# Performance work log

Measured on AMD Instinct MI355X. Metric: run time of the kernel, lower is better.

Reference implementation:

```python
import jax, jax.numpy as jnp
import numpy as np

D_MODEL = 1024
NUM_HEADS = 16
D_K = D_MODEL // NUM_HEADS
SCALE = 1.0 / np.sqrt(D_K).astype(np.float32)


def _rope_cos_sin(T, d_k):
    inv_freq = 1.0 / (10000.0 ** (jnp.arange(0, d_k, 2, dtype=jnp.float32) / d_k))
    t = jnp.arange(T, dtype=jnp.float32)
    freqs = jnp.outer(t, inv_freq)                      # [T, d_k/2]
    emb = jnp.concatenate([freqs, freqs], axis=-1)      # [T, d_k]
    return jnp.cos(emb)[None, None], jnp.sin(emb)[None, None]  # [1,1,T,d_k]


def _rotate_half(x):
    x1, x2 = x[..., : x.shape[-1] // 2], x[..., x.shape[-1] // 2 :]
    return jnp.concatenate([-x2, x1], axis=-1)


def setup_inputs() -> dict:
    key = jax.random.key(0)
    ks = jax.random.split(key, 8)
    B, T, C = 2, 2048, D_MODEL
    x = jax.random.normal(ks[0], (B, T, C), dtype=jnp.float32)
    # torch nn.Linear weights are [out, in]; forward does x @ W.T
    s = 1.0 / np.sqrt(C)
    Wq = jax.random.uniform(ks[1], (C, C), jnp.float32, -s, s)
    Wk = jax.random.uniform(ks[2], (C, C), jnp.float32, -s, s)
    Wv = jax.random.uniform(ks[3], (C, C), jnp.float32, -s, s)
    Wo = jax.random.uniform(ks[4], (C, C), jnp.float32, -s, s)
    bo = jax.random.uniform(ks[5], (C,), jnp.float32, -s, s)
    sector_bias = jnp.zeros((1, NUM_HEADS, 1, 1), dtype=jnp.float32)
    sector_weights = jax.random.uniform(ks[6], (B, T), jnp.float32, 0.5, 1.5)
    # causal mask, broadcastable to [B,H,T,T]; 0 -> masked
    mask = jnp.tril(jnp.ones((T, T), dtype=jnp.int32))[None, None]
    return {
        "x": x, "Wq": Wq, "Wk": Wk, "Wv": Wv, "Wo": Wo, "bo": bo,
        "sector_bias": sector_bias, "sector_weights": sector_weights,
        "mask": mask,
    }


def reference(x, Wq, Wk, Wv, Wo, bo, sector_bias, sector_weights, mask):
    B, T, C = x.shape
    H, dk = NUM_HEADS, D_K
    q = (x @ Wq.T).reshape(B, T, H, dk).transpose(0, 2, 1, 3)  # [B,H,T,dk]
    k = (x @ Wk.T).reshape(B, T, H, dk).transpose(0, 2, 1, 3)
    v = (x @ Wv.T).reshape(B, T, H, dk).transpose(0, 2, 1, 3)
    cos, sin = _rope_cos_sin(T, dk)
    q = q * cos + _rotate_half(q) * sin
    k = k * cos + _rotate_half(k) * sin
    scores = jnp.einsum("bhqd,bhkd->bhqk", q, k) * SCALE
    scores = scores + sector_bias
    scores = scores * sector_weights[:, None, None, :]  # broadcast over key dim
    scores = jnp.where(mask == 0, -jnp.inf, scores)
    attn = jax.nn.softmax(scores, axis=-1)
    out = jnp.einsum("bhqk,bhkd->bhqd", attn, v)
    out = out.transpose(0, 2, 1, 3).reshape(B, T, C)
    return out @ Wo.T + bo
```

## Files before the change

### kernel.cpp

```cpp
#include <hip/hip_runtime.h>


typedef __bf16 bf16x8 __attribute__((ext_vector_type(8)));
typedef float f32x4 __attribute__((ext_vector_type(4)));
typedef float f32x16 __attribute__((ext_vector_type(16)));
typedef unsigned short u16x8 __attribute__((ext_vector_type(8)));

__device__ __forceinline__ unsigned short f2bf(float f) {
    union { float f; unsigned int u; } c; c.f = f;
    unsigned int u = c.u;
    unsigned int r = u + 0x7fffu + ((u >> 16) & 1u);
    return (unsigned short)(r >> 16);
}
__device__ __forceinline__ unsigned cvtpk(float lo, float hi) {
    unsigned r;
    asm("v_cvt_pk_bf16_f32 %0, %1, %2" : "=v"(r) : "v"(lo), "v"(hi));
    return r;
}
__device__ __forceinline__ void plswap(unsigned a, unsigned b, unsigned& r0, unsigned& r1) {
#if __has_builtin(__builtin_amdgcn_permlane32_swap)
    auto s = __builtin_amdgcn_permlane32_swap(a, b, false, false);
    r0 = (unsigned)s[0]; r1 = (unsigned)s[1];
#else
    const int hh = (int)(threadIdx.x & 63) >> 5;
    const unsigned oa = (unsigned)__shfl_xor((int)a, 32);
    const unsigned ob = (unsigned)__shfl_xor((int)b, 32);
    r0 = hh ? ob : a;
    r1 = hh ? b : oa;
#endif
}
__device__ __forceinline__ void stage8_f32(unsigned short* dst, const float* src) {
    const float4 a = *(const float4*)src;
    const float4 b = *(const float4*)(src + 4);
    u16x8 v;
    v[0] = f2bf(a.x); v[1] = f2bf(a.y); v[2] = f2bf(a.z); v[3] = f2bf(a.w);
    v[4] = f2bf(b.x); v[5] = f2bf(b.y); v[6] = f2bf(b.z); v[7] = f2bf(b.w);
    *(u16x8*)dst = v;
}
__device__ __forceinline__ void async16(const unsigned short* g, unsigned short* l) {
    __builtin_amdgcn_global_load_lds(
        (const __attribute__((address_space(1))) void*)g,
        (__attribute__((address_space(3))) void*)l, 16, 0, 0);
}

__global__ __launch_bounds__(256) void cvt_all(
    const float* __restrict__ x, const float* __restrict__ Wq, const float* __restrict__ Wk,
    const float* __restrict__ Wv, const float* __restrict__ Wo,
    unsigned short* __restrict__ dst, int hasX, int n8)
{
    const int i = blockIdx.x * 256 + threadIdx.x;
    if (i >= n8) return;
    int r = i;
    const float* src; int off;
    const int xg = hasX ? 524288 : 0;
    if (r < xg) { src = x; off = r; }
    else {
        r -= xg;
        const int w = r >> 17, o = r & 131071;
        src = (w == 0) ? Wq : (w == 1) ? Wk : (w == 2) ? Wv : Wo;
        off = o;
    }
    stage8_f32(&dst[(size_t)i * 8], &src[(size_t)off * 8]);
}

template<int A_BF16>
__global__ __launch_bounds__(256) void gemm_qkv(
    const void* __restrict__ Av, const unsigned short* __restrict__ Wb,
    unsigned short* __restrict__ outv, const float* __restrict__ swg)
{
    constexpr int K = 1024, BK = 32;
    __shared__ __align__(16) unsigned short As[128 * BK];
    __shared__ __align__(16) unsigned short Bs[128 * BK];
    const int tid = threadIdx.x;
    const int wid = tid >> 6, lane = tid & 63, g = lane >> 4, l = lane & 15;
    const int wm = (wid & 1) * 64, wn = (wid >> 1) * 64;
    const int m0 = blockIdx.y * 128, n0 = blockIdx.x * 128;
    const int z = blockIdx.z;
    const unsigned short* W = Wb + (size_t)z * 1048576;

    f32x4 acc[4][4];
#pragma unroll
    for (int i = 0; i < 4; ++i)
#pragma unroll
        for (int j = 0; j < 4; ++j) acc[i][j] = f32x4{0.f, 0.f, 0.f, 0.f};

    const int r = tid >> 2;
    const int c = (tid & 3) * 8;
    unsigned short* AsW = &As[wid * 512];
    unsigned short* BsW = &Bs[wid * 512];

    for (int k0 = 0; k0 < K; k0 += BK) {
        __syncthreads();
        if (A_BF16) {
            const unsigned short* A = (const unsigned short*)Av;
            async16(&A[(size_t)(m0 + r) * K + k0 + c], AsW);
            async16(&A[(size_t)(m0 + 64 + r) * K + k0 + c], AsW + 2048);
        } else {
            const float* A = (const float*)Av;
            stage8_f32(&As[tid * 8],        &A[(size_t)(m0 + r) * K + k0 + c]);
            stage8_f32(&As[tid * 8 + 2048], &A[(size_t)(m0 + 64 + r) * K + k0 + c]);
        }
        async16(&W[(size_t)(n0 + r) * K + k0 + c], BsW);
        async16(&W[(size_t)(n0 + 64 + r) * K + k0 + c], BsW + 2048);
        __syncthreads();

        bf16x8 af[4], bfr[4];
#pragma unroll
        for (int im = 0; im < 4; ++im) af[im]  = *(const bf16x8*)&As[(wm + im * 16 + l) * BK + g * 8];
#pragma unroll
        for (int in = 0; in < 4; ++in) bfr[in] = *(const bf16x8*)&Bs[(wn + in * 16 + l) * BK + g * 8];
#pragma unroll
        for (int im = 0; im < 4; ++im)
#pragma unroll
            for (int in = 0; in < 4; ++in)
                acc[im][in] = __builtin_amdgcn_mfma_f32_16x16x32_bf16(af[im], bfr[in], acc[im][in], 0, 0, 0);
    }

    unsigned short* outq = outv + (size_t)z * 4194304;
    if (z < 2) {
        float freq[2];
#pragma unroll
        for (int in = 0; in < 2; ++in)
            freq[in] = exp2f(-(float)(in * 16 + l) * 0.41524101186f);
#pragma unroll
        for (int im = 0; im < 4; ++im)
#pragma unroll
            for (int i = 0; i < 4; ++i) {
                const int m = m0 + wm + im * 16 + g * 4 + i;
                const int b = m >> 11, t = m & 2047;
                float fw = 1.0f;
                if (z == 1) fw = 0.18033688011f * swg[(b << 11) + t];
#pragma unroll
                for (int in = 0; in < 2; ++in) {
                    const int n = n0 + wn + in * 16 + l;
                    const int h = n >> 6, d = n & 63;
                    const float ang = (float)t * freq[in];
                    const float cs = __cosf(ang), sn = __sinf(ang);
                    const float x1 = acc[im][in][i], x2 = acc[im][in + 2][i];
                    const size_t bidx = (((size_t)b * 16 + h) * 2048 + t) << 6;
                    outq[bidx + d]      = f2bf((x1 * cs - x2 * sn) * fw);
                    outq[bidx + d + 32] = f2bf((x2 * cs + x1 * sn) * fw);
                }
            }
    } else {
#pragma unroll
        for (int im = 0; im < 4; ++im)
#pragma unroll
            for (int in = 0; in < 4; ++in) {
                const int n = n0 + wn + in * 16 + l;
                const int h = n >> 6, d = n & 63;
                const int mb = m0 + wm + im * 16 + g * 4;
                const int bq = mb >> 11, t0 = mb & 2047;
                ushort4 pk;
                pk.x = f2bf(acc[im][in][0]); pk.y = f2bf(acc[im][in][1]);
                pk.z = f2bf(acc[im][in][2]); pk.w = f2bf(acc[im][in][3]);
                *(ushort4*)&outq[((size_t)(bq * 16 + h)) * 131072 + (size_t)d * 2048 + t0] = pk;
            }
    }
}

__global__ __launch_bounds__(256) void gemm_proj(
    const unsigned short* __restrict__ A, const unsigned short* __restrict__ W,
    float* __restrict__ out, const float* __restrict__ bias)
{
    constexpr int K = 1024, BK = 32;
    __shared__ __align__(16) unsigned short As[64 * BK];
    __shared__ __align__(16) unsigned short Bs[128 * BK];
    const int tid = threadIdx.x;
    const int wid = tid >> 6, lane = tid & 63, g = lane >> 4, l = lane & 15;
    const int wm = (wid & 1) * 32, wn = (wid >> 1) * 64;
    const int m0 = blockIdx.y * 64, n0 = blockIdx.x * 128;

    f32x4 acc[2][4];
#pragma unroll
    for (int i = 0; i < 2; ++i)
#pragma unroll
        for (int j = 0; j < 4; ++j) acc[i][j] = f32x4{0.f, 0.f, 0.f, 0.f};

    const int r = tid >> 2;
    const int c = (tid & 3) * 8;
    unsigned short* AsW = &As[wid * 512];
    unsigned short* BsW = &Bs[wid * 512];

    for (int k0 = 0; k0 < K; k0 += BK) {
        __syncthreads();
        async16(&A[(size_t)(m0 + r) * K + k0 + c], AsW);
        async16(&W[(size_t)(n0 + r) * K + k0 + c], BsW);
        async16(&W[(size_t)(n0 + 64 + r) * K + k0 + c], BsW + 2048);
        __syncthreads();

        bf16x8 af[2], bfr[4];
#pragma unroll
        for (int im = 0; im < 2; ++im) af[im]  = *(const bf16x8*)&As[(wm + im * 16 + l) * BK + g * 8];
#pragma unroll
        for (int in = 0; in < 4; ++in) bfr[in] = *(const bf16x8*)&Bs[(wn + in * 16 + l) * BK + g * 8];
#pragma unroll
        for (int im = 0; im < 2; ++im)
#pragma unroll
            for (int in = 0; in < 4; ++in)
                acc[im][in] = __builtin_amdgcn_mfma_f32_16x16x32_bf16(af[im], bfr[in], acc[im][in], 0, 0, 0);
    }

#pragma unroll
    for (int im = 0; im < 2; ++im)
#pragma unroll
        for (int in = 0; in < 4; ++in) {
            const int n = n0 + wn + in * 16 + l;
#pragma unroll
            for (int i = 0; i < 4; ++i) {
                const int m = m0 + wm + im * 16 + g * 4 + i;
                out[(size_t)m * 1024 + n] = acc[im][in][i] + bias[n];
            }
        }
}

__global__ __launch_bounds__(128, 2) void flash_attn(
    const unsigned short* __restrict__ Q, const unsigned short* __restrict__ Kg,
    const unsigned short* __restrict__ VT, const float* __restrict__ sbias,
    const float* __restrict__ sw, unsigned short* __restrict__ attn)
{
    constexpr int T = 2048;
    __shared__ __align__(16) unsigned short Mem[64 * 72 * 2];
    unsigned short* Ks  = Mem;
    unsigned short* VsT = Mem + 64 * 72;
    float* Cmb = (float*)Mem;

    const int tid = threadIdx.x, wid = tid >> 6, lane = tid & 63;
    const int hl = lane & 31, hh = lane >> 5;
    const int id = blockIdx.x;
    const int p  = 63 - (id >> 5);
    const int bh = id & 31, b = bh >> 4, h = bh & 15;
    const size_t base = (size_t)bh * T * 64;
    const size_t vtb  = (size_t)bh * 64 * T;
    const float bias = sbias[h];
    const float* swb = sw + b * T;

    bf16x8 onef;
#pragma unroll
    for (int j = 0; j < 8; ++j) onef[j] = (__bf16)1.0f;

    const int q0 = p * 32;
    bf16x8 qf[4];
#pragma unroll
    for (int ks = 0; ks < 4; ++ks)
        qf[ks] = *(const bf16x8*)&Q[base + (size_t)(q0 + hl) * 64 + ks * 16 + hh * 8];

    f32x16 oacc[2], lrow;
#pragma unroll
    for (int r = 0; r < 16; ++r) { oacc[0][r] = 0.f; oacc[1][r] = 0.f; lrow[r] = 0.f; }

    u16x8 kpre[4], vpre[4];
#pragma unroll
    for (int s = 0; s < 4; ++s) {
        const int ci = s * 128 + tid, rr = ci >> 3, c8 = (ci & 7) * 8;
        kpre[s] = *(const u16x8*)&Kg[base + (size_t)rr * 64 + c8];
        vpre[s] = *(const u16x8*)&VT[vtb + (size_t)rr * T + c8];
    }

    const int rounds = (p + 2) >> 1;
    for (int rd = 0; rd < rounds; ++rd) {
        const int k0 = rd * 64;
        __syncthreads();
#pragma unroll
        for (int s = 0; s < 4; ++s) {
            const int ci = s * 128 + tid, rr = ci >> 3, c8 = (ci & 7) * 8;
            *(u16x8*)&Ks[rr * 72 + c8]  = kpre[s];
            *(u16x8*)&VsT[rr * 72 + c8] = vpre[s];
        }
        __syncthreads();
        if (rd + 1 < rounds) {
            const int k1 = k0 + 64;
#pragma unroll
            for (int s = 0; s < 4; ++s) {
                const int ci = s * 128 + tid, rr = ci >> 3, c8 = (ci & 7) * 8;
                kpre[s] = *(const u16x8*)&Kg[base + (size_t)(k1 + rr) * 64 + c8];
                vpre[s] = *(const u16x8*)&VT[vtb + (size_t)rr * T + k1 + c8];
            }
        }

        const int kw0 = k0 + wid * 32;
        if (kw0 <= q0 + 31) {
            f32x16 sx;
#pragma unroll
            for (int r = 0; r < 16; ++r) sx[r] = 0.f;
#pragma unroll
            for (int ks = 0; ks < 4; ++ks) {
                const bf16x8 kf = *(const bf16x8*)&Ks[(wid * 32 + hl) * 72 + ks * 16 + hh * 8];
                sx = __builtin_amdgcn_mfma_f32_32x32x16_bf16(kf, qf[ks], sx, 0, 0, 0);
            }
            if (bias != 0.0f) {
                const float bn = bias * 1.44269504f;
#pragma unroll
                for (int r = 0; r < 16; ++r) {
                    const int kl = (r & 3) + 8 * (r >> 2) + 4 * hh;
                    sx[r] += bn * swb[kw0 + kl];
                }
            }
            if (kw0 + 31 > q0) {
                const int dq = q0 + hl - kw0;
#pragma unroll
                for (int r = 0; r < 16; ++r) {
                    const int kl = (r & 3) + 8 * (r >> 2) + 4 * hh;
                    sx[r] = (kl <= dq) ? sx[r] : -1e30f;
                }
            }
#pragma unroll
            for (int r = 0; r < 16; ++r) sx[r] = exp2f(sx[r]);

            unsigned wds[8];
#pragma unroll
            for (int g2 = 0; g2 < 4; ++g2) {
                wds[g2 * 2]     = cvtpk(sx[g2 * 4],     sx[g2 * 4 + 1]);
                wds[g2 * 2 + 1] = cvtpk(sx[g2 * 4 + 2], sx[g2 * 4 + 3]);
            }
            bf16x8 pf[2];
#pragma unroll
            for (int ks = 0; ks < 2; ++ks) {
                unsigned a0, a1, b0, b1;
                plswap(wds[4 * ks],     wds[4 * ks + 2], a0, a1);
                plswap(wds[4 * ks + 1], wds[4 * ks + 3], b0, b1);
                union { unsigned u[4]; bf16x8 v; } pk_;
                pk_.u[0] = a0; pk_.u[1] = b0;
                pk_.u[2] = a1; pk_.u[3] = b1;
                pf[ks] = pk_.v;
            }

            lrow = __builtin_amdgcn_mfma_f32_32x32x16_bf16(pf[0], onef, lrow, 0, 0, 0);
            lrow = __builtin_amdgcn_mfma_f32_32x32x16_bf16(pf[1], onef, lrow, 0, 0, 0);

#pragma unroll
            for (int ks = 0; ks < 2; ++ks)
#pragma unroll
                for (int dt = 0; dt < 2; ++dt) {
                    const bf16x8 vf = *(const bf16x8*)&VsT[(dt * 32 + hl) * 72 + wid * 32 + ks * 16 + hh * 8];
                    oacc[dt] = __builtin_amdgcn_mfma_f32_32x32x16_bf16(pf[ks], vf, oacc[dt], 0, 0, 0);
                }
        }
    }

    __syncthreads();
    if (wid == 1) {
#pragma unroll
        for (int dt = 0; dt < 2; ++dt)
#pragma unroll
            for (int r = 0; r < 16; ++r) Cmb[(dt * 16 + r) * 64 + lane] = oacc[dt][r];
#pragma unroll
        for (int r = 0; r < 16; ++r) Cmb[2048 + r * 64 + lane] = lrow[r];
    }
    __syncthreads();
    if (wid == 0) {
#pragma unroll
        for (int r = 0; r < 16; ++r) {
            const float li = 1.0f / (lrow[r] + Cmb[2048 + r * 64 + lane]);
            const int row = (r & 3) + 8 * (r >> 2) + 4 * hh;
            const int qr = q0 + row;
#pragma unroll
            for (int dt = 0; dt < 2; ++dt) {
                const float ov = oacc[dt][r] + Cmb[(dt * 16 + r) * 64 + lane];
                attn[(size_t)(b * T + qr) * 1024 + h * 64 + dt * 32 + hl] = f2bf(ov * li);
            }
        }
    }
}

extern "C" void kernel_launch(void* const* d_in, const int* in_sizes, int n_in,
                              void* d_out, int out_size, void* d_ws, size_t ws_size,
                              hipStream_t stream) {
    const float* x  = (const float*)d_in[0];
    const float* Wq = (const float*)d_in[1];
    const float* Wk = (const float*)d_in[2];
    const float* Wv = (const float*)d_in[3];
    const float* Wo = (const float*)d_in[4];
    const float* bo = (const float*)d_in[5];
    const float* sb = (const float*)d_in[6];
    const float* sw = (const float*)d_in[7];

    const size_t QKV_SZ = 4194304;
    const size_t W_SZ   = 1048576;
    unsigned short* ws16 = (unsigned short*)d_ws;
    const bool big = ws_size >= 2 * (4 * QKV_SZ + 4 * W_SZ);

    if (big) {
        unsigned short* xb    = ws16;
        unsigned short* Wb3   = xb + QKV_SZ;
        unsigned short* Wob   = Wb3 + 3 * W_SZ;
        unsigned short* qkv   = Wob + W_SZ;
        unsigned short* attnb = xb;

        cvt_all<<<4096, 256, 0, stream>>>(x, Wq, Wk, Wv, Wo, xb, 1, 1048576);
        gemm_qkv<1><<<dim3(8, 32, 3), 256, 0, stream>>>(xb, Wb3, qkv, sw);
        flash_attn<<<2048, 128, 0, stream>>>(qkv, qkv + QKV_SZ, qkv + 2 * QKV_SZ,
                                             sb, sw, attnb);
        gemm_proj<<<dim3(8, 64), 256, 0, stream>>>(attnb, Wob, (float*)d_out, bo);
    } else {
        unsigned short* qkv   = ws16;
        unsigned short* attnb = qkv + 3 * QKV_SZ;
        unsigned short* Wb3   = attnb;
        unsigned short* Wob   = qkv;

        cvt_all<<<1536, 256, 0, stream>>>(x, Wq, Wk, Wv, Wo, Wb3, 0, 393216);
        gemm_qkv<0><<<dim3(8, 32, 3), 256, 0, stream>>>(x, Wb3, qkv, sw);
        flash_attn<<<2048, 128, 0, stream>>>(qkv, qkv + QKV_SZ, qkv + 2 * QKV_SZ,
                                             sb, sw, attnb);
        cvt_all<<<512, 256, 0, stream>>>(x, Wo, Wo, Wo, Wo, Wob, 0, 131072);
        gemm_proj<<<dim3(8, 64), 256, 0, stream>>>(attnb, Wob, (float*)d_out, bo);
    }
}
```

Measured before the change: 205.8 us.

## Double-buffer LDS in QKV and projection GEMMs and remap blocks for XCD locality

Both GEMM kernels now use two LDS buffers, so the next K-tile is staged while MFMAs run on the current tile, leaving one barrier per iteration instead of two. Block indices are also remapped so that consecutive hardware-dispatched workgroups (round-robined across the 8 XCDs) land on neighbouring tiles, which should improve L2 reuse within each XCD. The cost is double the LDS footprint, which may reduce occupancy. With async loads, correctness depends on the vmcnt wait inside async16 and the barrier ordering.

```diff
diff --git a/kernel.cpp b/kernel.cpp
--- a/kernel.cpp
+++ b/kernel.cpp
@@ -69,13 +69,17 @@
     unsigned short* __restrict__ outv, const float* __restrict__ swg)
 {
     constexpr int K = 1024, BK = 32;
-    __shared__ __align__(16) unsigned short As[128 * BK];
-    __shared__ __align__(16) unsigned short Bs[128 * BK];
+    __shared__ __align__(16) unsigned short As[2][128 * BK];
+    __shared__ __align__(16) unsigned short Bs[2][128 * BK];
     const int tid = threadIdx.x;
     const int wid = tid >> 6, lane = tid & 63, g = lane >> 4, l = lane & 15;
     const int wm = (wid & 1) * 64, wn = (wid >> 1) * 64;
-    const int m0 = blockIdx.y * 128, n0 = blockIdx.x * 128;
-    const int z = blockIdx.z;
+
+    const int lin = blockIdx.x + (blockIdx.y << 3) + (blockIdx.z << 8);
+    const int wg  = (lin & 7) * 96 + (lin >> 3);
+    const int bx = wg & 7, by = (wg >> 3) & 31, bz = wg >> 8;
+    const int m0 = by * 128, n0 = bx * 128;
+    const int z = bz;
     const unsigned short* W = Wb + (size_t)z * 1048576;
 
     f32x4 acc[4][4];
@@ -86,34 +90,43 @@
 
     const int r = tid >> 2;
     const int c = (tid & 3) * 8;
-    unsigned short* AsW = &As[wid * 512];
-    unsigned short* BsW = &Bs[wid * 512];
-
-    for (int k0 = 0; k0 < K; k0 += BK) {
-        __syncthreads();
+
+    auto stage = [&](int buf, int k0) {
         if (A_BF16) {
             const unsigned short* A = (const unsigned short*)Av;
+            unsigned short* AsW = &As[buf][wid * 512];
             async16(&A[(size_t)(m0 + r) * K + k0 + c], AsW);
             async16(&A[(size_t)(m0 + 64 + r) * K + k0 + c], AsW + 2048);
         } else {
             const float* A = (const float*)Av;
-            stage8_f32(&As[tid * 8],        &A[(size_t)(m0 + r) * K + k0 + c]);
-            stage8_f32(&As[tid * 8 + 2048], &A[(size_t)(m0 + 64 + r) * K + k0 + c]);
-        }
+            stage8_f32(&As[buf][tid * 8],        &A[(size_t)(m0 + r) * K + k0 + c]);
+            stage8_f32(&As[buf][tid * 8 + 2048], &A[(size_t)(m0 + 64 + r) * K + k0 + c]);
+        }
+        unsigned short* BsW = &Bs[buf][wid * 512];
         async16(&W[(size_t)(n0 + r) * K + k0 + c], BsW);
         async16(&W[(size_t)(n0 + 64 + r) * K + k0 + c], BsW + 2048);
-        __syncthreads();
-
+    };
+
+    stage(0, 0);
+    __syncthreads();
+
+    for (int k0 = 0; k0 < K; k0 += BK) {
+        const int cur = (k0 >> 5) & 1;
+        if (k0 + BK < K) stage(cur ^ 1, k0 + BK);
+
+        const unsigned short* Asr = As[cur];
+        const unsigned short* Bsr = Bs[cur];
         bf16x8 af[4], bfr[4];
 #pragma unroll
-        for (int im = 0; im < 4; ++im) af[im]  = *(const bf16x8*)&As[(wm + im * 16 + l) * BK + g * 8];
-#pragma unroll
-        for (int in = 0; in < 4; ++in) bfr[in] = *(const bf16x8*)&Bs[(wn + in * 16 + l) * BK + g * 8];
+        for (int im = 0; im < 4; ++im) af[im]  = *(const bf16x8*)&Asr[(wm + im * 16 + l) * BK + g * 8];
+#pragma unroll
+        for (int in = 0; in < 4; ++in) bfr[in] = *(const bf16x8*)&Bsr[(wn + in * 16 + l) * BK + g * 8];
 #pragma unroll
         for (int im = 0; im < 4; ++im)
 #pragma unroll
             for (int in = 0; in < 4; ++in)
                 acc[im][in] = __builtin_amdgcn_mfma_f32_16x16x32_bf16(af[im], bfr[in], acc[im][in], 0, 0, 0);
+        __syncthreads();
     }
 
     unsigned short* outq = outv + (size_t)z * 4194304;
@@ -164,12 +177,15 @@
     float* __restrict__ out, const float* __restrict__ bias)
 {
     constexpr int K = 1024, BK = 32;
-    __shared__ __align__(16) unsigned short As[64 * BK];
-    __shared__ __align__(16) unsigned short Bs[128 * BK];
+    __shared__ __align__(16) unsigned short As[2][64 * BK];
+    __shared__ __align__(16) unsigned short Bs[2][128 * BK];
     const int tid = threadIdx.x;
     const int wid = tid >> 6, lane = tid & 63, g = lane >> 4, l = lane & 15;
     const int wm = (wid & 1) * 32, wn = (wid >> 1) * 64;
-    const int m0 = blockIdx.y * 64, n0 = blockIdx.x * 128;
+
+    const int lin = blockIdx.x + (blockIdx.y << 3);
+    const int wg  = (lin & 7) * 64 + (lin >> 3);
+    const int m0 = (wg >> 3) * 64, n0 = (wg & 7) * 128;
 
     f32x4 acc[2][4];
 #pragma unroll
@@ -179,26 +195,35 @@
 
     const int r = tid >> 2;
     const int c = (tid & 3) * 8;
-    unsigned short* AsW = &As[wid * 512];
-    unsigned short* BsW = &Bs[wid * 512];
-
-    for (int k0 = 0; k0 < K; k0 += BK) {
-        __syncthreads();
+
+    auto stage = [&](int buf, int k0) {
+        unsigned short* AsW = &As[buf][wid * 512];
+        unsigned short* BsW = &Bs[buf][wid * 512];
         async16(&A[(size_t)(m0 + r) * K + k0 + c], AsW);
         async16(&W[(size_t)(n0 + r) * K + k0 + c], BsW);
         async16(&W[(size_t)(n0 + 64 + r) * K + k0 + c], BsW + 2048);
-        __syncthreads();
-
+    };
+
+    stage(0, 0);
+    __syncthreads();
+
+    for (int k0 = 0; k0 < K; k0 += BK) {
+        const int cur = (k0 >> 5) & 1;
+        if (k0 + BK < K) stage(cur ^ 1, k0 + BK);
+
+        const unsigned short* Asr = As[cur];
+        const unsigned short* Bsr = Bs[cur];
         bf16x8 af[2], bfr[4];
 #pragma unroll
-        for (int im = 0; im < 2; ++im) af[im]  = *(const bf16x8*)&As[(wm + im * 16 + l) * BK + g * 8];
-#pragma unroll
-        for (int in = 0; in < 4; ++in) bfr[in] = *(const bf16x8*)&Bs[(wn + in * 16 + l) * BK + g * 8];
+        for (int im = 0; im < 2; ++im) af[im]  = *(const bf16x8*)&Asr[(wm + im * 16 + l) * BK + g * 8];
+#pragma unroll
+        for (int in = 0; in < 4; ++in) bfr[in] = *(const bf16x8*)&Bsr[(wn + in * 16 + l) * BK + g * 8];
 #pragma unroll
         for (int im = 0; im < 2; ++im)
 #pragma unroll
             for (int in = 0; in < 4; ++in)
                 acc[im][in] = __builtin_amdgcn_mfma_f32_16x16x32_bf16(af[im], bfr[in], acc[im][in], 0, 0, 0);
+        __syncthreads();
     }
 
 #pragma unroll
```

Result: faster. 198.5 us (-3.5%).
